# Kernel tuning notes

Measured on AMD Instinct MI355X. Metric: run time of the kernel, lower is better.

Reference implementation:

```python
import jax, jax.numpy as jnp
import numpy as np

B, S, DIM = 4, 512, 2048
E, INTER = 32, 1024
G, TOPK_G, TOPK = 8, 4, 6
ROUTE_SCALE = 2.5
SHARED_INTER = 2 * INTER  # n_shared_experts * moe_inter_dim


def setup_inputs() -> dict:
    key = jax.random.key(0)
    ks = jax.random.split(key, 8)
    sd = 0.02
    return {
        "x": jax.random.normal(ks[0], (B, S, DIM), jnp.float32),
        "gate_w": jax.random.normal(ks[1], (E, DIM), jnp.float32) * sd,
        "w11": jax.random.normal(ks[2], (E, INTER, DIM), jnp.float32) * sd,  # gate proj (torch Linear weight [out,in])
        "w33": jax.random.normal(ks[3], (E, INTER, DIM), jnp.float32) * sd,  # up proj
        "w22": jax.random.normal(ks[4], (E, DIM, INTER), jnp.float32) * sd,  # down proj
        "sw1": jax.random.normal(ks[5], (SHARED_INTER, DIM), jnp.float32) * sd,
        "sw2": jax.random.normal(ks[6], (DIM, SHARED_INTER), jnp.float32) * sd,
        "sw3": jax.random.normal(ks[7], (SHARED_INTER, DIM), jnp.float32) * sd,
    }


def _gate(xf, gate_w):
    # sigmoid scores, group-limited greedy top-k (bias=None branch)
    scores = jax.nn.sigmoid(xf @ gate_w.T)                      # [T, E]
    gs = scores.reshape(-1, G, E // G)                          # [T, G, E/G]
    group_scores = gs.max(axis=-1)                              # amax since bias is None
    _, gidx = jax.lax.top_k(group_scores, TOPK_G)               # [T, TOPK_G]
    gmask = jnp.any(jnp.arange(G)[None, None, :] == gidx[:, :, None], axis=1)  # [T, G] keep-mask
    masked = jnp.where(gmask[:, :, None], gs, -jnp.inf).reshape(-1, E)
    _, idx = jax.lax.top_k(masked, TOPK)                        # [T, TOPK]
    w = jnp.take_along_axis(scores, idx, axis=1)                # gather from original (pre-mask) scores
    w = w / jnp.sum(w, axis=-1, keepdims=True) * ROUTE_SCALE    # sigmoid normalization + route_scale
    return w, idx


def reference(x, gate_w, w11, w33, w22, sw1, sw2, sw3):
    xf = x.reshape(-1, DIM)                                     # [T, D]
    T = xf.shape[0]
    w, idx = _gate(xf, gate_w)
    # dense combine weights: equals the gather->gmm->scatter*prob of the original
    c = jnp.zeros((T, E), xf.dtype).at[jnp.arange(T)[:, None], idx].add(w)  # [T, E]
    g = jnp.einsum('td,eid->tei', xf, w11)                      # fc1 (gate)
    u = jnp.einsum('td,eid->tei', xf, w33)                      # fc2 (up)
    act = jax.nn.silu(g) * u                                    # fused SiLU gating
    y = jnp.einsum('tei,te,edi->td', act, c, w22)               # down proj + weighted combine
    shared = (jax.nn.silu(xf @ sw1.T) * (xf @ sw3.T)) @ sw2.T   # shared experts MLP
    return (y + shared).reshape(x.shape)
```

## Files before the change

### kernel.cpp

```cpp
#include <hip/hip_runtime.h>
#include <hip/hip_bf16.h>

#define T_TOK  2048
#define DIMSZ  2048
#define NEXP   32
#define INTERS 1024
#define SINTER 2048
#define NTOPK  6

typedef __bf16 bf16x8 __attribute__((ext_vector_type(8)));
typedef float  f32x4  __attribute__((ext_vector_type(4)));
typedef unsigned short u16x8 __attribute__((ext_vector_type(8)));

__device__ __forceinline__ unsigned short f2b(float f) {
    __hip_bfloat16 h = __float2bfloat16(f);
    return __builtin_bit_cast(unsigned short, h);
}

__device__ __forceinline__ void gl_lds16(const unsigned short* g, unsigned short* l) {
    __builtin_amdgcn_global_load_lds(
        (const __attribute__((address_space(1))) void*)g,
        (__attribute__((address_space(3))) void*)l, 16, 0, 0);
}

struct CvtJobs {
    const float4*   src[7];
    unsigned short* dst[7];
    int             n8[7];
};
__global__ __launch_bounds__(256) void cvt_multi(CvtJobs jobs) {
    const int gtid = blockIdx.x * blockDim.x + threadIdx.x;
    const int gstride = gridDim.x * blockDim.x;
    #pragma unroll
    for (int j = 0; j < 7; ++j) {
        const float4* __restrict__ s = jobs.src[j];
        unsigned short* __restrict__ d = jobs.dst[j];
        const int n8 = jobs.n8[j];
        for (int i = gtid; i < n8; i += gstride) {
            float4 a = s[2 * i];
            float4 b = s[2 * i + 1];
            u16x8 o;
            o[0] = f2b(a.x); o[1] = f2b(a.y); o[2] = f2b(a.z); o[3] = f2b(a.w);
            o[4] = f2b(b.x); o[5] = f2b(b.y); o[6] = f2b(b.z); o[7] = f2b(b.w);
            *(u16x8*)&d[(size_t)i * 8] = o;
        }
    }
}

__global__ void cvt_f2b(const float4* __restrict__ src, ushort4* __restrict__ dst, int n4) {
    int stride = gridDim.x * blockDim.x;
    for (int i = blockIdx.x * blockDim.x + threadIdx.x; i < n4; i += stride) {
        float4 v = src[i];
        ushort4 o;
        o.x = f2b(v.x); o.y = f2b(v.y); o.z = f2b(v.z); o.w = f2b(v.w);
        dst[i] = o;
    }
}

#define SCT 8
#define SCK 128
__global__ __launch_bounds__(256) void gate_scores_kernel(
    const float* __restrict__ x, const float* __restrict__ gw, float* __restrict__ scores)
{
    __shared__ float xs[SCT * SCK];
    __shared__ float gs[NEXP * (SCK + 1)];
    const int t0 = blockIdx.x * SCT;
    const int tid = threadIdx.x;
    const int tl = tid >> 5, e = tid & 31;
    float acc = 0.f;
    for (int k0 = 0; k0 < DIMSZ; k0 += SCK) {
        {
            int row = tid >> 5, d4 = tid & 31;
            *(float4*)&xs[row * SCK + d4 * 4] =
                *(const float4*)&x[(size_t)(t0 + row) * DIMSZ + k0 + d4 * 4];
        }
        #pragma unroll
        for (int i = 0; i < 4; ++i) {
            int lin = tid + i * 256;
            int row = lin >> 5, d4 = lin & 31;
            float4 v = *(const float4*)&gw[(size_t)row * DIMSZ + k0 + d4 * 4];
            float* dst = &gs[row * (SCK + 1) + d4 * 4];
            dst[0] = v.x; dst[1] = v.y; dst[2] = v.z; dst[3] = v.w;
        }
        __syncthreads();
        #pragma unroll 8
        for (int d = 0; d < SCK; ++d)
            acc += xs[tl * SCK + d] * gs[e * (SCK + 1) + d];
        __syncthreads();
    }
    scores[(size_t)(t0 + tl) * NEXP + e] = 1.f / (1.f + expf(-acc));
}

__global__ __launch_bounds__(256) void topk_kernel(
    const float* __restrict__ scores,
    int* __restrict__ counts, int* __restrict__ toklist, float* __restrict__ wgts)
{
    int t = blockIdx.x * 256 + threadIdx.x;
    if (t >= T_TOK) return;
    float sc[NEXP];
    #pragma unroll
    for (int e = 0; e < NEXP; ++e) sc[e] = scores[(size_t)t * NEXP + e];

    float gsc[8];
    #pragma unroll
    for (int g = 0; g < 8; ++g) {
        float m = sc[4 * g];
        #pragma unroll
        for (int j = 1; j < 4; ++j) m = fmaxf(m, sc[4 * g + j]);
        gsc[g] = m;
    }
    bool gsel[8] = {false, false, false, false, false, false, false, false};
    for (int it = 0; it < 4; ++it) {
        int bi = -1; float bv = -1e30f;
        #pragma unroll
        for (int g = 0; g < 8; ++g)
            if (!gsel[g] && gsc[g] > bv) { bv = gsc[g]; bi = g; }
        gsel[bi] = true;
    }
    bool esel[NEXP];
    #pragma unroll
    for (int e = 0; e < NEXP; ++e) esel[e] = false;
    int   idx[NTOPK];
    float w[NTOPK];
    float sum = 0.f;
    for (int it = 0; it < NTOPK; ++it) {
        int bi = -1; float bv = -1e30f;
        #pragma unroll
        for (int e = 0; e < NEXP; ++e) {
            if (!gsel[e >> 2] || esel[e]) continue;
            if (sc[e] > bv) { bv = sc[e]; bi = e; }
        }
        esel[bi] = true; idx[it] = bi; w[it] = bv; sum += bv;
    }
    float scale = 2.5f / sum;
    for (int k = 0; k < NTOPK; ++k) {
        int e = idx[k];
        int s = atomicAdd(&counts[e], 1);
        toklist[e * T_TOK + s] = (t << 3) | k;
        wgts[e * T_TOK + s]   = w[k] * scale;
    }
}

__global__ __launch_bounds__(256, 2) void fc1_all(
    const unsigned short* __restrict__ A,
    const unsigned short* __restrict__ w11b, const unsigned short* __restrict__ w33b,
    const unsigned short* __restrict__ sw1b, const unsigned short* __restrict__ sw3b,
    unsigned short* __restrict__ h, unsigned short* __restrict__ hs,
    const int* __restrict__ counts, const int* __restrict__ toklist)
{
    constexpr int BM = 128, BN = 128, BK = 64, LDK = 64, K = DIMSZ;
    __shared__ unsigned short As[BM * LDK];
    __shared__ unsigned short B1s[BN * LDK];
    __shared__ unsigned short B2s[BN * LDK];
    __shared__ int aRowS[BM];
    __shared__ int cRowS[BM];
    __shared__ int map[4];

    const int tid = threadIdx.x;
    if (tid == 0) {
        const int wgid = blockIdx.x;
        if (wgid < 256) {
            map[0] = 1; map[1] = NEXP; map[2] = wgid >> 4; map[3] = wgid & 15;
        } else {
            const int rid = wgid - 256;
            const int xt = rid & 7, ty = rid >> 3;
            int acc2 = 0, fe = -1, fy = 0;
            #pragma unroll
            for (int e2 = 0; e2 < NEXP; ++e2) {
                const int nt = (counts[e2] + 127) >> 7;
                if (fe < 0 && ty < acc2 + nt) { fe = e2; fy = ty - acc2; }
                acc2 += nt;
            }
            map[0] = 0; map[1] = fe; map[2] = fy; map[3] = xt;
        }
    }
    __syncthreads();
    const bool SH = (map[0] != 0);
    const int e  = map[1];
    if (!SH && e < 0) return;
    const int m0 = map[2] * BM;
    const int n0 = map[3] * BN;
    const int N  = SH ? SINTER : INTERS;
    const int M  = SH ? T_TOK : counts[e];

    const size_t eoff = SH ? 0 : (size_t)e * INTERS * DIMSZ;
    const unsigned short* B1 = (SH ? sw1b : w11b) + eoff;
    const unsigned short* B2 = (SH ? sw3b : w33b) + eoff;
    unsigned short* Hout = SH ? hs : h;

    if (tid < BM) {
        int r = m0 + tid;
        if (SH) { aRowS[tid] = r; cRowS[tid] = r; }
        else if (r < M) {
            int ent = toklist[e * T_TOK + r];
            int t = ent >> 3, k = ent & 7;
            aRowS[tid] = t; cRowS[tid] = t * NTOPK + k;
        } else { aRowS[tid] = 0; cRowS[tid] = -1; }
    }
    __syncthreads();

    f32x4 acc1[4][4] = {};
    f32x4 acc2v[4][4] = {};

    const int wave = tid >> 6;
    const int lane = tid & 63;
    const int wm = (wave >> 1) * 64;
    const int wn = (wave & 1) * 64;
    const int lm = lane & 15;
    const int quad = lane >> 4;

    const unsigned short *aP[4], *b1P[4], *b2P[4];
    {
        const int l8 = lane >> 3;
        const int sg = (lane & 7) ^ l8;
        #pragma unroll
        for (int i = 0; i < 4; ++i) {
            const int c = wave * 4 + i;
            const int r = c * 8 + l8;
            aP[i]  = A  + (size_t)aRowS[r] * K + sg * 8;
            b1P[i] = B1 + (size_t)(n0 + r) * K + sg * 8;
            b2P[i] = B2 + (size_t)(n0 + r) * K + sg * 8;
        }
    }

    for (int k0 = 0; k0 < K; k0 += BK) {
        #pragma unroll
        for (int i = 0; i < 4; ++i) {
            const int c = wave * 4 + i;
            gl_lds16(aP[i]  + k0, &As [c * 512]);
            gl_lds16(b1P[i] + k0, &B1s[c * 512]);
            gl_lds16(b2P[i] + k0, &B2s[c * 512]);
        }
        __syncthreads();
        #pragma unroll
        for (int kh = 0; kh < 2; ++kh) {
            const int soff = (((kh << 2) | quad) ^ (lm & 7)) << 3;
            bf16x8 af[4], bf1[4], bf2[4];
            #pragma unroll
            for (int ti = 0; ti < 4; ++ti)
                af[ti] = *(const bf16x8*)&As[(wm + ti * 16 + lm) * LDK + soff];
            #pragma unroll
            for (int tj = 0; tj < 4; ++tj) {
                bf1[tj] = *(const bf16x8*)&B1s[(wn + tj * 16 + lm) * LDK + soff];
                bf2[tj] = *(const bf16x8*)&B2s[(wn + tj * 16 + lm) * LDK + soff];
            }
            #pragma unroll
            for (int ti = 0; ti < 4; ++ti)
                #pragma unroll
                for (int tj = 0; tj < 4; ++tj) {
                    acc1[ti][tj] = __builtin_amdgcn_mfma_f32_16x16x32_bf16(
                        af[ti], bf1[tj], acc1[ti][tj], 0, 0, 0);
                    acc2v[ti][tj] = __builtin_amdgcn_mfma_f32_16x16x32_bf16(
                        af[ti], bf2[tj], acc2v[ti][tj], 0, 0, 0);
                }
        }
        __syncthreads();
    }

    #pragma unroll
    for (int ti = 0; ti < 4; ++ti) {
        #pragma unroll
        for (int r = 0; r < 4; ++r) {
            int lrow = wm + ti * 16 + quad * 4 + r;
            int cr = cRowS[lrow];
            if (cr < 0) continue;
            #pragma unroll
            for (int tj = 0; tj < 4; ++tj) {
                int nn = n0 + wn + tj * 16 + lm;
                float g = acc1[ti][tj][r];
                float u = acc2v[ti][tj][r];
                float hv = g / (1.f + expf(-g)) * u;
                Hout[(size_t)cr * N + nn] = f2b(hv);
            }
        }
    }
}

__global__ __launch_bounds__(256, 2) void fc2_all(
    const unsigned short* __restrict__ h, const unsigned short* __restrict__ hs,
    const unsigned short* __restrict__ w22b, const unsigned short* __restrict__ sw2b,
    float* __restrict__ yexp, float* __restrict__ out,
    const int* __restrict__ counts, const int* __restrict__ toklist,
    const float* __restrict__ wgts)
{
    constexpr int BM = 128, BN = 128, BK = 64, LDK = 64;
    __shared__ unsigned short As[BM * LDK];
    __shared__ unsigned short Bs[BN * LDK];
    __shared__ int   aRowS[BM];
    __shared__ int   cRowS[BM];
    __shared__ float cWS[BM];
    __shared__ int   map[4];

    const int tid = threadIdx.x;
    if (tid == 0) {
        const int wgid = blockIdx.x;
        if (wgid < 256) {
            map[0] = 1; map[1] = NEXP; map[2] = wgid >> 4; map[3] = wgid & 15;
        } else {
            const int rid = wgid - 256;
            const int xt = rid & 15, ty = rid >> 4;
            int acc2 = 0, fe = -1, fy = 0;
            #pragma unroll
            for (int e2 = 0; e2 < NEXP; ++e2) {
                const int nt = (counts[e2] + 127) >> 7;
                if (fe < 0 && ty < acc2 + nt) { fe = e2; fy = ty - acc2; }
                acc2 += nt;
            }
            map[0] = 0; map[1] = fe; map[2] = fy; map[3] = xt;
        }
    }
    __syncthreads();
    const bool SH = (map[0] != 0);
    const int e  = map[1];
    if (!SH && e < 0) return;
    const int m0 = map[2] * BM;
    const int n0 = map[3] * BN;
    const int K  = SH ? SINTER : INTERS;
    const int M  = SH ? T_TOK : counts[e];

    const unsigned short* Asrc = SH ? hs : h;
    const unsigned short* B = SH ? sw2b : (w22b + (size_t)e * DIMSZ * INTERS);
    float* C = SH ? out : yexp;

    if (tid < BM) {
        int r = m0 + tid;
        if (SH) { aRowS[tid] = r; cRowS[tid] = r; cWS[tid] = 1.f; }
        else if (r < M) {
            int ent = toklist[e * T_TOK + r];
            int slot = (ent >> 3) * NTOPK + (ent & 7);
            aRowS[tid] = slot; cRowS[tid] = slot;
            cWS[tid] = wgts[e * T_TOK + r];
        } else { aRowS[tid] = 0; cRowS[tid] = -1; cWS[tid] = 0.f; }
    }
    __syncthreads();

    f32x4 acc[4][4] = {};

    const int wave = tid >> 6;
    const int lane = tid & 63;
    const int wm = (wave >> 1) * 64;
    const int wn = (wave & 1) * 64;
    const int lm = lane & 15;
    const int quad = lane >> 4;

    const unsigned short *aP[4], *bP[4];
    {
        const int l8 = lane >> 3;
        const int sg = (lane & 7) ^ l8;
        #pragma unroll
        for (int i = 0; i < 4; ++i) {
            const int c = wave * 4 + i;
            const int r = c * 8 + l8;
            aP[i] = Asrc + (size_t)aRowS[r] * K + sg * 8;
            bP[i] = B    + (size_t)(n0 + r) * K + sg * 8;
        }
    }

    for (int k0 = 0; k0 < K; k0 += BK) {
        #pragma unroll
        for (int i = 0; i < 4; ++i) {
            const int c = wave * 4 + i;
            gl_lds16(aP[i] + k0, &As[c * 512]);
            gl_lds16(bP[i] + k0, &Bs[c * 512]);
        }
        __syncthreads();
        #pragma unroll
        for (int kh = 0; kh < 2; ++kh) {
            const int soff = (((kh << 2) | quad) ^ (lm & 7)) << 3;
            bf16x8 af[4], bfr[4];
            #pragma unroll
            for (int ti = 0; ti < 4; ++ti)
                af[ti] = *(const bf16x8*)&As[(wm + ti * 16 + lm) * LDK + soff];
            #pragma unroll
            for (int tj = 0; tj < 4; ++tj)
                bfr[tj] = *(const bf16x8*)&Bs[(wn + tj * 16 + lm) * LDK + soff];
            #pragma unroll
            for (int ti = 0; ti < 4; ++ti)
                #pragma unroll
                for (int tj = 0; tj < 4; ++tj)
                    acc[ti][tj] = __builtin_amdgcn_mfma_f32_16x16x32_bf16(
                        af[ti], bfr[tj], acc[ti][tj], 0, 0, 0);
        }
        __syncthreads();
    }

    #pragma unroll
    for (int ti = 0; ti < 4; ++ti) {
        #pragma unroll
        for (int r = 0; r < 4; ++r) {
            int lrow = wm + ti * 16 + quad * 4 + r;
            int cr = cRowS[lrow];
            if (cr < 0) continue;
            #pragma unroll
            for (int tj = 0; tj < 4; ++tj) {
                int nn = n0 + wn + tj * 16 + lm;
                C[(size_t)cr * DIMSZ + nn] = acc[ti][tj][r] * cWS[lrow];
            }
        }
    }
}

__global__ __launch_bounds__(256) void combine_kernel(
    const float4* __restrict__ yexp, float4* __restrict__ out, int n4)
{
    const int D4 = DIMSZ / 4;
    int stride = gridDim.x * blockDim.x;
    for (int i = blockIdx.x * blockDim.x + threadIdx.x; i < n4; i += stride) {
        int t = i / D4, d4 = i - t * D4;
        const float4* r = yexp + (size_t)t * NTOPK * D4 + d4;
        float4 a = out[i];
        #pragma unroll
        for (int k = 0; k < NTOPK; ++k) {
            float4 s = r[(size_t)k * D4];
            a.x += s.x; a.y += s.y; a.z += s.z; a.w += s.w;
        }
        out[i] = a;
    }
}

template <bool GROUPED>
__global__ __launch_bounds__(256) void fc1_fb(
    const unsigned short* __restrict__ A,
    const float* __restrict__ B1t, const float* __restrict__ B2t,
    unsigned short* __restrict__ H, int N, int K, int M_fixed,
    const int* __restrict__ counts, const int* __restrict__ toklist)
{
    constexpr int BM = 128, BN = 128, BK = 64, LDK = 72;
    __shared__ unsigned short As[BM * LDK];
    __shared__ unsigned short B1s[BN * LDK];
    __shared__ unsigned short B2s[BN * LDK];
    __shared__ int aRowS[BM];
    __shared__ int cRowS[BM];

    const int tid = threadIdx.x;
    const int e  = blockIdx.z;
    const int m0 = blockIdx.y * BM;
    const int n0 = blockIdx.x * BN;

    int M;
    const float *B1, *B2;
    if constexpr (GROUPED) {
        M = counts[e];
        if (m0 >= M) return;
        B1 = B1t + (size_t)e * N * K;
        B2 = B2t + (size_t)e * N * K;
    } else { M = M_fixed; B1 = B1t; B2 = B2t; }

    if (tid < BM) {
        int r = m0 + tid;
        if constexpr (GROUPED) {
            if (r < M) {
                int ent = toklist[e * T_TOK + r];
                int t = ent >> 3, k = ent & 7;
                aRowS[tid] = t; cRowS[tid] = t * NTOPK + k;
            } else { aRowS[tid] = 0; cRowS[tid] = -1; }
        } else { aRowS[tid] = r; cRowS[tid] = (r < M) ? r : -1; }
    }
    __syncthreads();

    f32x4 acc1[4][4] = {};
    f32x4 acc2[4][4] = {};
    const int wave = tid >> 6, lane = tid & 63;
    const int wm = (wave >> 1) * 64, wn = (wave & 1) * 64;
    const int lm = lane & 15, quad = lane >> 4;

    for (int k0 = 0; k0 < K; k0 += BK) {
        #pragma unroll
        for (int i = 0; i < 4; ++i) {
            int lin = tid + i * 256;
            int row = lin >> 3, cq = lin & 7;
            *(float4*)&As[row * LDK + cq * 8] =
                *(const float4*)(A + (size_t)aRowS[row] * K + k0 + cq * 8);
        }
        #pragma unroll
        for (int i = 0; i < 8; ++i) {
            int lin = tid + i * 256;
            int row = lin >> 4, cq = lin & 15;
            size_t boff = (size_t)(n0 + row) * K + k0 + cq * 4;
            float4 v1 = *(const float4*)(B1 + boff);
            float4 v2 = *(const float4*)(B2 + boff);
            ushort4 o1, o2;
            o1.x = f2b(v1.x); o1.y = f2b(v1.y); o1.z = f2b(v1.z); o1.w = f2b(v1.w);
            o2.x = f2b(v2.x); o2.y = f2b(v2.y); o2.z = f2b(v2.z); o2.w = f2b(v2.w);
            *(ushort4*)&B1s[row * LDK + cq * 4] = o1;
            *(ushort4*)&B2s[row * LDK + cq * 4] = o2;
        }
        __syncthreads();
        #pragma unroll
        for (int kk = 0; kk < BK; kk += 32) {
            bf16x8 af[4], b1f[4], b2f[4];
            #pragma unroll
            for (int ti = 0; ti < 4; ++ti)
                af[ti] = *(const bf16x8*)&As[(wm + ti * 16 + lm) * LDK + kk + quad * 8];
            #pragma unroll
            for (int tj = 0; tj < 4; ++tj) {
                b1f[tj] = *(const bf16x8*)&B1s[(wn + tj * 16 + lm) * LDK + kk + quad * 8];
                b2f[tj] = *(const bf16x8*)&B2s[(wn + tj * 16 + lm) * LDK + kk + quad * 8];
            }
            #pragma unroll
            for (int ti = 0; ti < 4; ++ti)
                #pragma unroll
                for (int tj = 0; tj < 4; ++tj) {
                    acc1[ti][tj] = __builtin_amdgcn_mfma_f32_16x16x32_bf16(
                        af[ti], b1f[tj], acc1[ti][tj], 0, 0, 0);
                    acc2[ti][tj] = __builtin_amdgcn_mfma_f32_16x16x32_bf16(
                        af[ti], b2f[tj], acc2[ti][tj], 0, 0, 0);
                }
        }
        __syncthreads();
    }

    #pragma unroll
    for (int ti = 0; ti < 4; ++ti) {
        #pragma unroll
        for (int r = 0; r < 4; ++r) {
            int lrow = wm + ti * 16 + quad * 4 + r;
            int cr = cRowS[lrow];
            if (cr < 0) continue;
            #pragma unroll
            for (int tj = 0; tj < 4; ++tj) {
                int nn = n0 + wn + tj * 16 + lm;
                float g = acc1[ti][tj][r];
                float u = acc2[ti][tj][r];
                float hv = g / (1.f + expf(-g)) * u;
                H[(size_t)cr * N + nn] = f2b(hv);
            }
        }
    }
}

#define SHARED_F32  1
#define GROUP_FC2   3

template <int MODE>
__global__ __launch_bounds__(256) void gemm_fb(
    const unsigned short* __restrict__ A, const float* __restrict__ Bt,
    float* __restrict__ Cf, int N, int K, int M_fixed,
    const int* __restrict__ counts, const int* __restrict__ toklist,
    const float* __restrict__ wgts)
{
    constexpr int BM = 128, BN = 128, BK = 64, LDK = 72;
    __shared__ unsigned short As[BM * LDK];
    __shared__ unsigned short Bs[BN * LDK];
    __shared__ int   aRowS[BM];
    __shared__ int   cRowS[BM];
    __shared__ float cWS[BM];

    const int tid = threadIdx.x;
    const int e  = blockIdx.z;
    const int m0 = blockIdx.y * BM;
    const int n0 = blockIdx.x * BN;

    int M;
    const float* B;
    if constexpr (MODE == GROUP_FC2) {
        M = counts[e];
        if (m0 >= M) return;
        B = Bt + (size_t)e * N * K;
    } else { M = M_fixed; B = Bt; }

    if (tid < BM) {
        int r = m0 + tid;
        if constexpr (MODE == GROUP_FC2) {
            if (r < M) {
                int ent = toklist[e * T_TOK + r];
                int t = ent >> 3, k = ent & 7;
                aRowS[tid] = t * NTOPK + k; cRowS[tid] = t;
                cWS[tid] = wgts[e * T_TOK + r];
            } else { aRowS[tid] = 0; cRowS[tid] = -1; cWS[tid] = 0.f; }
        } else { aRowS[tid] = r; cRowS[tid] = (r < M) ? r : -1; cWS[tid] = 0.f; }
    }
    __syncthreads();

    f32x4 acc[4][4] = {};
    const int wave = tid >> 6, lane = tid & 63;
    const int wm = (wave >> 1) * 64, wn = (wave & 1) * 64;
    const int lm = lane & 15, quad = lane >> 4;

    for (int k0 = 0; k0 < K; k0 += BK) {
        #pragma unroll
        for (int i = 0; i < 4; ++i) {
            int lin = tid + i * 256;
            int row = lin >> 3, cq = lin & 7;
            *(float4*)&As[row * LDK + cq * 8] =
                *(const float4*)(A + (size_t)aRowS[row] * K + k0 + cq * 8);
        }
        #pragma unroll
        for (int i = 0; i < 8; ++i) {
            int lin = tid + i * 256;
            int row = lin >> 4, cq = lin & 15;
            float4 v = *(const float4*)(B + (size_t)(n0 + row) * K + k0 + cq * 4);
            ushort4 o;
            o.x = f2b(v.x); o.y = f2b(v.y); o.z = f2b(v.z); o.w = f2b(v.w);
            *(ushort4*)&Bs[row * LDK + cq * 4] = o;
        }
        __syncthreads();
        #pragma unroll
        for (int kk = 0; kk < BK; kk += 32) {
            bf16x8 af[4], bfr[4];
            #pragma unroll
            for (int ti = 0; ti < 4; ++ti)
                af[ti] = *(const bf16x8*)&As[(wm + ti * 16 + lm) * LDK + kk + quad * 8];
            #pragma unroll
            for (int tj = 0; tj < 4; ++tj)
                bfr[tj] = *(const bf16x8*)&Bs[(wn + tj * 16 + lm) * LDK + kk + quad * 8];
            #pragma unroll
            for (int ti = 0; ti < 4; ++ti)
                #pragma unroll
                for (int tj = 0; tj < 4; ++tj)
                    acc[ti][tj] = __builtin_amdgcn_mfma_f32_16x16x32_bf16(
                        af[ti], bfr[tj], acc[ti][tj], 0, 0, 0);
        }
        __syncthreads();
    }

    #pragma unroll
    for (int ti = 0; ti < 4; ++ti) {
        #pragma unroll
        for (int r = 0; r < 4; ++r) {
            int lrow = wm + ti * 16 + quad * 4 + r;
            int cr = cRowS[lrow];
            if (cr < 0) continue;
            #pragma unroll
            for (int tj = 0; tj < 4; ++tj) {
                int nn = n0 + wn + tj * 16 + lm;
                float v = acc[ti][tj][r];
                if constexpr (MODE == SHARED_F32)
                    Cf[(size_t)cr * N + nn] = v;
                else
                    atomicAdd(&Cf[(size_t)cr * N + nn], v * cWS[lrow]);
            }
        }
    }
}

extern "C" void kernel_launch(void* const* d_in, const int* in_sizes, int n_in,
                              void* d_out, int out_size, void* d_ws, size_t ws_size,
                              hipStream_t stream)
{
    const float* x   = (const float*)d_in[0];
    const float* gw  = (const float*)d_in[1];
    const float* w11 = (const float*)d_in[2];
    const float* w33 = (const float*)d_in[3];
    const float* w22 = (const float*)d_in[4];
    const float* sw1 = (const float*)d_in[5];
    const float* sw2 = (const float*)d_in[6];
    const float* sw3 = (const float*)d_in[7];
    float* out = (float*)d_out;

    char* ws = (char*)d_ws;
    size_t off = 0;
    auto alloc = [&](size_t b) { void* p = ws + off; off = (off + b + 255) & ~(size_t)255; return p; };
    int*            counts  = (int*)alloc(NEXP * 4);
    int*            toklist = (int*)alloc((size_t)NEXP * T_TOK * 4);
    float*          wgts    = (float*)alloc((size_t)NEXP * T_TOK * 4);
    float*          scores  = (float*)alloc((size_t)T_TOK * NEXP * 4);
    unsigned short* xb      = (unsigned short*)alloc((size_t)T_TOK * DIMSZ * 2);
    unsigned short* h       = (unsigned short*)alloc((size_t)T_TOK * NTOPK * INTERS * 2);
    unsigned short* hs      = (unsigned short*)alloc((size_t)T_TOK * SINTER * 2);

    const size_t nW = (size_t)NEXP * INTERS * DIMSZ;
    const size_t nS = (size_t)SINTER * DIMSZ;
    const size_t yBytes = (size_t)T_TOK * NTOPK * DIMSZ * 4;
    const size_t needed = 3 * (nW * 2) + 3 * (nS * 2) + yBytes + 8 * 256;
    const bool FAST = (off + needed) <= ws_size;

    hipMemsetAsync(counts, 0, NEXP * 4, stream);

    const int n4x = T_TOK * DIMSZ / 4;

    if (FAST) {
        unsigned short* w11b = (unsigned short*)alloc(nW * 2);
        unsigned short* w33b = (unsigned short*)alloc(nW * 2);
        unsigned short* w22b = (unsigned short*)alloc(nW * 2);
        unsigned short* sw1b = (unsigned short*)alloc(nS * 2);
        unsigned short* sw3b = (unsigned short*)alloc(nS * 2);
        unsigned short* sw2b = (unsigned short*)alloc(nS * 2);
        float*          yexp = (float*)alloc(yBytes);

        CvtJobs jobs;
        jobs.src[0] = (const float4*)x;   jobs.dst[0] = xb;   jobs.n8[0] = (int)((size_t)T_TOK * DIMSZ / 8);
        jobs.src[1] = (const float4*)w11; jobs.dst[1] = w11b; jobs.n8[1] = (int)(nW / 8);
        jobs.src[2] = (const float4*)w33; jobs.dst[2] = w33b; jobs.n8[2] = (int)(nW / 8);
        jobs.src[3] = (const float4*)w22; jobs.dst[3] = w22b; jobs.n8[3] = (int)(nW / 8);
        jobs.src[4] = (const float4*)sw1; jobs.dst[4] = sw1b; jobs.n8[4] = (int)(nS / 8);
        jobs.src[5] = (const float4*)sw3; jobs.dst[5] = sw3b; jobs.n8[5] = (int)(nS / 8);
        jobs.src[6] = (const float4*)sw2; jobs.dst[6] = sw2b; jobs.n8[6] = (int)(nS / 8);
        cvt_multi<<<4096, 256, 0, stream>>>(jobs);

        gate_scores_kernel<<<T_TOK / SCT, 256, 0, stream>>>(x, gw, scores);
        topk_kernel<<<(T_TOK + 255) / 256, 256, 0, stream>>>(scores, counts, toklist, wgts);

        fc1_all<<<256 + 128 * 8, 256, 0, stream>>>(
            xb, w11b, w33b, sw1b, sw3b, h, hs, counts, toklist);
        fc2_all<<<256 + 128 * 16, 256, 0, stream>>>(
            h, hs, w22b, sw2b, yexp, out, counts, toklist, wgts);
        combine_kernel<<<2048, 256, 0, stream>>>((const float4*)yexp, (float4*)out, n4x);
    } else {
        cvt_f2b<<<4096, 256, 0, stream>>>((const float4*)x, (ushort4*)xb, n4x);
        gate_scores_kernel<<<T_TOK / SCT, 256, 0, stream>>>(x, gw, scores);
        topk_kernel<<<(T_TOK + 255) / 256, 256, 0, stream>>>(scores, counts, toklist, wgts);

        fc1_fb<false><<<dim3(SINTER / 128, T_TOK / 128, 1), 256, 0, stream>>>(
            xb, sw1, sw3, hs, SINTER, DIMSZ, T_TOK, nullptr, nullptr);
        gemm_fb<SHARED_F32><<<dim3(DIMSZ / 128, T_TOK / 128, 1), 256, 0, stream>>>(
            hs, sw2, out, DIMSZ, SINTER, T_TOK, nullptr, nullptr, nullptr);
        fc1_fb<true><<<dim3(INTERS / 128, T_TOK / 128, NEXP), 256, 0, stream>>>(
            xb, w11, w33, h, INTERS, DIMSZ, 0, counts, toklist);
        gemm_fb<GROUP_FC2><<<dim3(DIMSZ / 128, T_TOK / 128, NEXP), 256, 0, stream>>>(
            h, w22, out, DIMSZ, INTERS, 0, counts, toklist, wgts);
    }
}
```

Measured before the change: 1.221 ms.

## Overlap down-proj weight conversion with fc1 GEMM via interleaved converter workgroups

```diff
diff --git a/kernel.cpp b/kernel.cpp
--- a/kernel.cpp
+++ b/kernel.cpp
@@ -8,6 +8,9 @@
 #define SINTER 2048
 #define NTOPK  6
 
+#define N8_W   ((32 * 1024 * 2048) / 8)
+#define N8_S   ((2048 * 2048) / 8)
+
 typedef __bf16 bf16x8 __attribute__((ext_vector_type(8)));
 typedef float  f32x4  __attribute__((ext_vector_type(4)));
 typedef unsigned short u16x8 __attribute__((ext_vector_type(8)));
@@ -23,28 +26,46 @@
         (__attribute__((address_space(3))) void*)l, 16, 0, 0);
 }
 
-struct CvtJobs {
-    const float4*   src[7];
-    unsigned short* dst[7];
-    int             n8[7];
+__device__ __forceinline__ void cvt_stream(
+    const float4* __restrict__ s, unsigned short* __restrict__ d,
+    int n8, int i0, int stride)
+{
+    int i = i0;
+    for (; i + stride < n8; i += 2 * stride) {
+        const int i2 = i + stride;
+        float4 a0 = s[2 * (size_t)i];
+        float4 b0 = s[2 * (size_t)i + 1];
+        float4 a1 = s[2 * (size_t)i2];
+        float4 b1 = s[2 * (size_t)i2 + 1];
+        u16x8 o0, o1;
+        o0[0] = f2b(a0.x); o0[1] = f2b(a0.y); o0[2] = f2b(a0.z); o0[3] = f2b(a0.w);
+        o0[4] = f2b(b0.x); o0[5] = f2b(b0.y); o0[6] = f2b(b0.z); o0[7] = f2b(b0.w);
+        o1[0] = f2b(a1.x); o1[1] = f2b(a1.y); o1[2] = f2b(a1.z); o1[3] = f2b(a1.w);
+        o1[4] = f2b(b1.x); o1[5] = f2b(b1.y); o1[6] = f2b(b1.z); o1[7] = f2b(b1.w);
+        *(u16x8*)&d[(size_t)i * 8]  = o0;
+        *(u16x8*)&d[(size_t)i2 * 8] = o1;
+    }
+    if (i < n8) {
+        float4 a = s[2 * (size_t)i];
+        float4 b = s[2 * (size_t)i + 1];
+        u16x8 o;
+        o[0] = f2b(a.x); o[1] = f2b(a.y); o[2] = f2b(a.z); o[3] = f2b(a.w);
+        o[4] = f2b(b.x); o[5] = f2b(b.y); o[6] = f2b(b.z); o[7] = f2b(b.w);
+        *(u16x8*)&d[(size_t)i * 8] = o;
+    }
+}
+
+struct CvtJobs5 {
+    const float4*   src[5];
+    unsigned short* dst[5];
+    int             n8[5];
 };
-__global__ __launch_bounds__(256) void cvt_multi(CvtJobs jobs) {
+__global__ __launch_bounds__(256) void cvt_multi5(CvtJobs5 jobs) {
     const int gtid = blockIdx.x * blockDim.x + threadIdx.x;
     const int gstride = gridDim.x * blockDim.x;
     #pragma unroll
-    for (int j = 0; j < 7; ++j) {
-        const float4* __restrict__ s = jobs.src[j];
-        unsigned short* __restrict__ d = jobs.dst[j];
-        const int n8 = jobs.n8[j];
-        for (int i = gtid; i < n8; i += gstride) {
-            float4 a = s[2 * i];
-            float4 b = s[2 * i + 1];
-            u16x8 o;
-            o[0] = f2b(a.x); o[1] = f2b(a.y); o[2] = f2b(a.z); o[3] = f2b(a.w);
-            o[4] = f2b(b.x); o[5] = f2b(b.y); o[6] = f2b(b.z); o[7] = f2b(b.w);
-            *(u16x8*)&d[(size_t)i * 8] = o;
-        }
-    }
+    for (int j = 0; j < 5; ++j)
+        cvt_stream(jobs.src[j], jobs.dst[j], jobs.n8[j], gtid, gstride);
 }
 
 __global__ void cvt_f2b(const float4* __restrict__ src, ushort4* __restrict__ dst, int n4) {
@@ -146,7 +167,9 @@
     const unsigned short* __restrict__ w11b, const unsigned short* __restrict__ w33b,
     const unsigned short* __restrict__ sw1b, const unsigned short* __restrict__ sw3b,
     unsigned short* __restrict__ h, unsigned short* __restrict__ hs,
-    const int* __restrict__ counts, const int* __restrict__ toklist)
+    const int* __restrict__ counts, const int* __restrict__ toklist,
+    const float* __restrict__ w22f, const float* __restrict__ sw2f,
+    unsigned short* __restrict__ w22b, unsigned short* __restrict__ sw2b)
 {
     constexpr int BM = 128, BN = 128, BK = 64, LDK = 64, K = DIMSZ;
     __shared__ unsigned short As[BM * LDK];
@@ -162,20 +185,33 @@
         if (wgid < 256) {
             map[0] = 1; map[1] = NEXP; map[2] = wgid >> 4; map[3] = wgid & 15;
         } else {
-            const int rid = wgid - 256;
-            const int xt = rid & 7, ty = rid >> 3;
-            int acc2 = 0, fe = -1, fy = 0;
-            #pragma unroll
-            for (int e2 = 0; e2 < NEXP; ++e2) {
-                const int nt = (counts[e2] + 127) >> 7;
-                if (fe < 0 && ty < acc2 + nt) { fe = e2; fy = ty - acc2; }
-                acc2 += nt;
+            const int r = wgid - 256;
+            if ((r % 3) == 2) {
+                map[0] = 2; map[1] = r / 3; map[2] = 0; map[3] = 0;
+            } else {
+                const int rid = r - (r + 1) / 3;
+                const int xt = rid & 7, ty = rid >> 3;
+                int acc2 = 0, fe = -1, fy = 0;
+                #pragma unroll
+                for (int e2 = 0; e2 < NEXP; ++e2) {
+                    const int nt = (counts[e2] + 127) >> 7;
+                    if (fe < 0 && ty < acc2 + nt) { fe = e2; fy = ty - acc2; }
+                    acc2 += nt;
+                }
+                map[0] = 0; map[1] = fe; map[2] = fy; map[3] = xt;
             }
-            map[0] = 0; map[1] = fe; map[2] = fy; map[3] = xt;
         }
     }
     __syncthreads();
-    const bool SH = (map[0] != 0);
+    const int role = map[0];
+    if (role == 2) {
+        const int i0 = map[1] * 256 + tid;
+        const int stride = 512 * 256;
+        cvt_stream((const float4*)w22f, w22b, N8_W, i0, stride);
+        cvt_stream((const float4*)sw2f, sw2b, N8_S, i0, stride);
+        return;
+    }
+    const bool SH = (role == 1);
     const int e  = map[1];
     if (!SH && e < 0) return;
     const int m0 = map[2] * BM;
@@ -678,21 +714,20 @@
         unsigned short* sw2b = (unsigned short*)alloc(nS * 2);
         float*          yexp = (float*)alloc(yBytes);
 
-        CvtJobs jobs;
+        CvtJobs5 jobs;
         jobs.src[0] = (const float4*)x;   jobs.dst[0] = xb;   jobs.n8[0] = (int)((size_t)T_TOK * DIMSZ / 8);
         jobs.src[1] = (const float4*)w11; jobs.dst[1] = w11b; jobs.n8[1] = (int)(nW / 8);
         jobs.src[2] = (const float4*)w33; jobs.dst[2] = w33b; jobs.n8[2] = (int)(nW / 8);
-        jobs.src[3] = (const float4*)w22; jobs.dst[3] = w22b; jobs.n8[3] = (int)(nW / 8);
-        jobs.src[4] = (const float4*)sw1; jobs.dst[4] = sw1b; jobs.n8[4] = (int)(nS / 8);
-        jobs.src[5] = (const float4*)sw3; jobs.dst[5] = sw3b; jobs.n8[5] = (int)(nS / 8);
-        jobs.src[6] = (const float4*)sw2; jobs.dst[6] = sw2b; jobs.n8[6] = (int)(nS / 8);
-        cvt_multi<<<4096, 256, 0, stream>>>(jobs);
+        jobs.src[3] = (const float4*)sw1; jobs.dst[3] = sw1b; jobs.n8[3] = (int)(nS / 8);
+        jobs.src[4] = (const float4*)sw3; jobs.dst[4] = sw3b; jobs.n8[4] = (int)(nS / 8);
+        cvt_multi5<<<4096, 256, 0, stream>>>(jobs);
 
         gate_scores_kernel<<<T_TOK / SCT, 256, 0, stream>>>(x, gw, scores);
         topk_kernel<<<(T_TOK + 255) / 256, 256, 0, stream>>>(scores, counts, toklist, wgts);
 
-        fc1_all<<<256 + 128 * 8, 256, 0, stream>>>(
-            xb, w11b, w33b, sw1b, sw3b, h, hs, counts, toklist);
+        fc1_all<<<256 + 1536, 256, 0, stream>>>(
+            xb, w11b, w33b, sw1b, sw3b, h, hs, counts, toklist,
+            w22, sw2, w22b, sw2b);
         fc2_all<<<256 + 128 * 16, 256, 0, stream>>>(
             h, hs, w22b, sw2b, yexp, out, counts, toklist, wgts);
         combine_kernel<<<2048, 256, 0, stream>>>((const float4*)yexp, (float4*)out, n4x);
```

New measurement: 1.165 ms. 1.05x faster.
